# Optimization experiments

Measured on AMD Instinct MI355X. Metric: run time of the kernel, lower is better.

## Reference

```python
import jax, jax.numpy as jnp
import numpy as np

DIM = 96       # d_model / channels
DSTATE = 16    # SSM state size N
DINNER = 2 * DIM   # expand=2 -> 192
DTRANK = 6     # ceil(DIM/16)
K = 4          # scan directions
B, H, W = 2, 56, 56


def _ln(x, g, b, eps=1e-5):
    m = x.mean(-1, keepdims=True)
    v = x.var(-1, keepdims=True)
    return (x - m) * jax.lax.rsqrt(v + eps) * g + b


def _dwconv3(x, w, b):  # x [B,C,H,W], w [C,1,3,3] depthwise, SAME padding
    y = jax.lax.conv_general_dilated(x, w, (1, 1), [(1, 1), (1, 1)],
                                     feature_group_count=x.shape[1],
                                     dimension_numbers=('NCHW', 'OIHW', 'NCHW'))
    return y + b[None, :, None, None]


def _bn(x, g, b, m, v, eps=1e-5):  # eval-mode BatchNorm2d on NCHW
    inv = jax.lax.rsqrt(v + eps)
    return (x - m[None, :, None, None]) * (inv * g)[None, :, None, None] + b[None, :, None, None]


def _selective_scan(u, dt, A, Bs, Cs, Dp, dt_bias):
    # u, dt: [B,K,D,L]; A: [K,D,N]; Bs,Cs: [B,K,N,L]; Dp, dt_bias: [K,D]
    dt = jax.nn.softplus(dt + dt_bias[None, :, :, None])
    dA = jnp.exp(jnp.einsum('bkdl,kdn->lbkdn', dt, A))           # [L,B,K,D,N]
    dBu = jnp.einsum('bkdl,bknl,bkdl->lbkdn', dt, Bs, u)          # [L,B,K,D,N]
    Ct = jnp.moveaxis(Cs, -1, 0)                                  # [L,B,K,N]
    h0 = jnp.zeros(dA.shape[1:], dA.dtype)

    def step(h, inp):
        dA_l, dBu_l, C_l = inp
        h = dA_l * h + dBu_l
        return h, jnp.einsum('bkdn,bkn->bkd', h, C_l)

    _, ys = jax.lax.scan(step, h0, (dA, dBu, Ct))                 # ys [L,B,K,D]
    return jnp.moveaxis(ys, 0, -1) + u * Dp[None, :, :, None]     # [B,K,D,L]


def setup_inputs() -> dict:
    key = jax.random.key(0)
    ks = jax.random.split(key, 12)
    s = 0.02
    f32 = jnp.float32
    inp = {}
    inp['x'] = jax.random.normal(ks[0], (B, H, W, DIM), f32)
    # conv branch: depthwise 3x3 + BN + ReLU + 1x1 + BN
    inp['dw_w'] = jax.random.normal(ks[1], (DIM, 1, 3, 3), f32) * s
    inp['dw_b'] = jnp.zeros((DIM,), f32)
    inp['bn1_g'] = jnp.ones((DIM,), f32); inp['bn1_b'] = jnp.zeros((DIM,), f32)
    inp['bn1_m'] = jnp.zeros((DIM,), f32); inp['bn1_v'] = jnp.ones((DIM,), f32)
    inp['pw_w'] = jax.random.normal(ks[2], (DIM, DIM), f32) * s
    inp['pw_b'] = jnp.zeros((DIM,), f32)
    inp['bn2_g'] = jnp.ones((DIM,), f32); inp['bn2_b'] = jnp.zeros((DIM,), f32)
    inp['bn2_m'] = jnp.zeros((DIM,), f32); inp['bn2_v'] = jnp.ones((DIM,), f32)
    # pre-mamba LayerNorm
    inp['ln_g'] = jnp.ones((DIM,), f32); inp['ln_b'] = jnp.zeros((DIM,), f32)
    # SS2D params
    inp['in_proj_w'] = jax.random.normal(ks[3], (2 * DINNER, DIM), f32) * s
    inp['conv_w'] = jax.random.normal(ks[4], (DINNER, 1, 3, 3), f32) * s
    inp['conv_b'] = jnp.zeros((DINNER,), f32)
    inp['x_proj_w'] = jax.random.normal(ks[5], (K, DTRANK + 2 * DSTATE, DINNER), f32) * s
    inp['dt_w'] = jax.random.normal(ks[6], (K, DINNER, DTRANK), f32) * s
    inp['dt_b'] = jnp.full((K, DINNER), -4.6, f32)  # softplus(dt_b) ~= 0.01
    inp['A_logs'] = jnp.log(jnp.tile(jnp.arange(1, DSTATE + 1, dtype=f32), (K * DINNER, 1)))
    inp['Ds'] = jnp.ones((K * DINNER,), f32)
    inp['out_norm_g'] = jnp.ones((DINNER,), f32); inp['out_norm_b'] = jnp.zeros((DINNER,), f32)
    inp['out_proj_w'] = jax.random.normal(ks[7], (DIM, DINNER), f32) * s
    # fusion: Linear(2*dim, dim) + LayerNorm(dim)
    inp['fus_w'] = jax.random.normal(ks[8], (DIM, 2 * DIM), f32) * s
    inp['fus_b'] = jnp.zeros((DIM,), f32)
    inp['fus_ln_g'] = jnp.ones((DIM,), f32); inp['fus_ln_b'] = jnp.zeros((DIM,), f32)
    return inp


def reference(x, dw_w, dw_b, bn1_g, bn1_b, bn1_m, bn1_v, pw_w, pw_b,
              bn2_g, bn2_b, bn2_m, bn2_v, ln_g, ln_b,
              in_proj_w, conv_w, conv_b, x_proj_w, dt_w, dt_b, A_logs, Ds,
              out_norm_g, out_norm_b, out_proj_w, fus_w, fus_b, fus_ln_g, fus_ln_b):
    Bsz, Hh, Ww, C = x.shape
    L = Hh * Ww
    # ----- conv branch -----
    xc = jnp.transpose(x, (0, 3, 1, 2))                       # [B,C,H,W]
    c = jax.nn.relu(_bn(_dwconv3(xc, dw_w, dw_b), bn1_g, bn1_b, bn1_m, bn1_v))
    c = jnp.einsum('bchw,oc->bohw', c, pw_w) + pw_b[None, :, None, None]
    conv_out = jnp.transpose(_bn(c, bn2_g, bn2_b, bn2_m, bn2_v), (0, 2, 3, 1))
    # ----- mamba (SS2D) branch -----
    xn = _ln(x, ln_g, ln_b)
    xz = xn @ in_proj_w.T                                     # [B,H,W,2*Din]
    xm, z = jnp.split(xz, 2, axis=-1)
    xm = jnp.transpose(xm, (0, 3, 1, 2))                      # [B,Din,H,W]
    xm = jax.nn.silu(_dwconv3(xm, conv_w, conv_b))
    v1 = xm.reshape(Bsz, DINNER, L)                           # row-major scan
    v2 = jnp.transpose(xm, (0, 1, 3, 2)).reshape(Bsz, DINNER, L)  # col-major scan
    xs = jnp.stack([v1, v2, v1[..., ::-1], v2[..., ::-1]], axis=1)  # [B,4,Din,L]
    x_dbl = jnp.einsum('bkdl,kcd->bkcl', xs, x_proj_w)
    dts, Bmat, Cmat = jnp.split(x_dbl, [DTRANK, DTRANK + DSTATE], axis=2)
    dts = jnp.einsum('bkrl,kdr->bkdl', dts, dt_w)
    A = -jnp.exp(A_logs).reshape(K, DINNER, DSTATE)
    out_y = _selective_scan(xs, dts, A, Bmat, Cmat, Ds.reshape(K, DINNER), dt_b)
    y1 = out_y[:, 0]
    inv_y = out_y[:, 2:4][..., ::-1]
    y2 = inv_y[:, 0]
    y3 = jnp.transpose(inv_y[:, 1].reshape(Bsz, DINNER, Ww, Hh), (0, 1, 3, 2)).reshape(Bsz, DINNER, L)
    y4 = jnp.transpose(out_y[:, 1].reshape(Bsz, DINNER, Ww, Hh), (0, 1, 3, 2)).reshape(Bsz, DINNER, L)
    y = jnp.transpose(y1 + y2 + y3 + y4, (0, 2, 1)).reshape(Bsz, Hh, Ww, DINNER)
    y = _ln(y, out_norm_g, out_norm_b)
    y = y * jax.nn.silu(z)
    mamba_out = y @ out_proj_w.T                              # [B,H,W,C]
    # ----- fusion + residual -----
    fused = jnp.concatenate([conv_out, mamba_out], axis=-1) @ fus_w.T + fus_b
    fused = _ln(fused, fus_ln_g, fus_ln_b)
    return x + fused
```

## Files before the change

kernel.cpp:

```cpp
#include <hip/hip_runtime.h>
#include <math.h>

#define BZ 2
#define HH 56
#define WW 56
#define LL 3136
#define CC 96
#define DI 192
#define NS 16
#define RR 6
#define NT 49
#define NCH 98
#define CH 32

#define OFF_CONV   0
#define OFF_XMRAW  602112
#define OFF_Z      1806336
#define OFF_V1     3010560
#define OFF_V2     4214784
#define OFF_DT     5419008
#define OFF_BS     10235904
#define OFF_CS     10637312
#define OFF_Y      11038720
#define OFF_Y13    15855616
#define OFF_T      18264064
#define OFF_W2     19468288

__device__ __forceinline__ float softplusf(float x) {
    if (x > 20.f) return x;
    return log1pf(__expf(x));
}

__global__ __launch_bounds__(64) void k0_w2(const float* __restrict__ fus_w,
                                            const float* __restrict__ opw,
                                            float* __restrict__ W2) {
    int i = blockIdx.x * 64 + threadIdx.x;
    if (i >= CC * DI) return;
    int o = i / DI, d = i % DI;
    float acc = 0.f;
    for (int j = 0; j < CC; ++j)
        acc += fus_w[o * DI + CC + j] * opw[j * DI + d];
    W2[i] = acc;
}

__global__ __launch_bounds__(256) void k0c_negA(const float* __restrict__ A_logs,
                                                float* __restrict__ negA) {
    int i = blockIdx.x * 256 + threadIdx.x;
    if (i < 4 * DI * NS) negA[i] = -__expf(A_logs[i]);
}

__global__ __launch_bounds__(256) void k1a_dw(const float* __restrict__ x,
    const float* __restrict__ dw_w, const float* __restrict__ dw_b,
    const float* __restrict__ bn1_g, const float* __restrict__ bn1_b,
    const float* __restrict__ bn1_m, const float* __restrict__ bn1_v,
    float* __restrict__ cbuf) {
    int i = blockIdx.x * 256 + threadIdx.x;
    if (i >= BZ * LL * CC) return;
    int c = i % CC;
    int bl = i / CC;
    int l = bl % LL, b = bl / LL;
    int h = l / WW, w = l % WW;
    float acc = dw_b[c];
    #pragma unroll
    for (int dy = -1; dy <= 1; ++dy) {
        int hh = h + dy; if (hh < 0 || hh >= HH) continue;
        #pragma unroll
        for (int dx = -1; dx <= 1; ++dx) {
            int ww = w + dx; if (ww < 0 || ww >= WW) continue;
            acc += x[((b * HH + hh) * WW + ww) * CC + c] * dw_w[c * 9 + (dy + 1) * 3 + (dx + 1)];
        }
    }
    float inv = rsqrtf(bn1_v[c] + 1e-5f);
    float v = (acc - bn1_m[c]) * inv * bn1_g[c] + bn1_b[c];
    cbuf[i] = fmaxf(v, 0.f);
}

__global__ __launch_bounds__(256) void k1b_pw(const float* __restrict__ cbuf,
    const float* __restrict__ pw_w, const float* __restrict__ pw_b,
    const float* __restrict__ bn2_g, const float* __restrict__ bn2_b,
    const float* __restrict__ bn2_m, const float* __restrict__ bn2_v,
    float* __restrict__ conv_out) {
    int t0 = blockIdx.x * 64;
    int b = blockIdx.y;
    int lane = threadIdx.x & 63;
    int wvu = __builtin_amdgcn_readfirstlane(threadIdx.x >> 6);
    __shared__ float ct[CC * 65];
    __shared__ float res[64 * 97];
    const float* cb = cbuf + (b * LL + t0) * CC;
    for (int e = threadIdx.x; e < 64 * CC; e += 256) {
        int p = e / CC, c = e % CC;
        ct[c * 65 + p] = cb[e];
    }
    __syncthreads();
    float acc[24];
    const float* pb = pw_b + wvu * 24;
    #pragma unroll
    for (int j = 0; j < 24; ++j) acc[j] = pb[j];
    const float* wb = pw_w + (wvu * 24) * CC;
    for (int c = 0; c < CC; ++c) {
        float xv = ct[c * 65 + lane];
        #pragma unroll
        for (int j = 0; j < 24; ++j)
            acc[j] += xv * wb[j * CC + c];
    }
    #pragma unroll
    for (int j = 0; j < 24; ++j) {
        int o = wvu * 24 + j;
        float inv = rsqrtf(bn2_v[o] + 1e-5f);
        res[lane * 97 + o] = (acc[j] - bn2_m[o]) * inv * bn2_g[o] + bn2_b[o];
    }
    __syncthreads();
    float* ob = conv_out + (b * LL + t0) * CC;
    for (int e = threadIdx.x; e < 64 * CC; e += 256) {
        int pl = e / CC, o = e % CC;
        ob[e] = res[pl * 97 + o];
    }
}

__global__ __launch_bounds__(256) void k2_inproj(const float* __restrict__ x,
    const float* __restrict__ ln_g, const float* __restrict__ ln_b,
    const float* __restrict__ ipw,
    float* __restrict__ xm_raw, float* __restrict__ z_buf) {
    int t0 = blockIdx.x * 64;
    int og = blockIdx.y;
    int b = blockIdx.z;
    int lane = threadIdx.x & 63;
    int wv = threadIdx.x >> 6;
    int wvu = __builtin_amdgcn_readfirstlane(wv);
    __shared__ float xt[64 * 97];
    __shared__ float xn[96 * 65];
    __shared__ float ps[4][64], ps2[4][64];
    const float* xb = x + (b * LL + t0) * CC;
    for (int e = threadIdx.x; e < 64 * CC; e += 256) {
        int p = e / CC, c = e % CC;
        xt[p * 97 + c] = xb[e];
    }
    __syncthreads();
    float s = 0.f, s2 = 0.f;
    #pragma unroll
    for (int j = 0; j < 24; ++j) {
        float v = xt[lane * 97 + wvu * 24 + j];
        s += v; s2 += v * v;
    }
    ps[wv][lane] = s; ps2[wv][lane] = s2;
    __syncthreads();
    float st = 0.f, st2 = 0.f;
    #pragma unroll
    for (int i = 0; i < 4; ++i) { st += ps[i][lane]; st2 += ps2[i][lane]; }
    float m = st * (1.f / 96.f);
    float inv = rsqrtf(st2 * (1.f / 96.f) - m * m + 1e-5f);
    #pragma unroll
    for (int j = 0; j < 24; ++j) {
        int c = wvu * 24 + j;
        xn[c * 65 + lane] = (xt[lane * 97 + c] - m) * inv * ln_g[c] + ln_b[c];
    }
    __syncthreads();
    float acc[24];
    #pragma unroll
    for (int j = 0; j < 24; ++j) acc[j] = 0.f;
    const float* wbase = ipw + (og * 96 + wvu * 24) * CC;
    for (int c = 0; c < CC; ++c) {
        float xv = xn[c * 65 + lane];
        #pragma unroll
        for (int j = 0; j < 24; ++j)
            acc[j] += xv * wbase[j * CC + c];
    }
    int p = t0 + lane;
    #pragma unroll
    for (int j = 0; j < 24; ++j) {
        int out = og * 96 + wvu * 24 + j;
        if (out < DI) xm_raw[(b * DI + out) * LL + p] = acc[j];
        else          z_buf[(b * DI + (out - DI)) * LL + p] = acc[j];
    }
}

__global__ __launch_bounds__(256) void k3_dw(const float* __restrict__ xm_raw,
    const float* __restrict__ conv_w, const float* __restrict__ conv_b,
    float* __restrict__ v1, float* __restrict__ v2) {
    int bd = blockIdx.x;
    int half = blockIdx.y;
    int d = bd % DI;
    int h0 = half * 28;
    __shared__ float tile[28 * 57];
    const float* src = xm_raw + bd * LL;
    float wloc[9];
    #pragma unroll
    for (int i = 0; i < 9; ++i) wloc[i] = conv_w[d * 9 + i];
    float bias = conv_b[d];
    for (int e = threadIdx.x; e < 28 * WW; e += 256) {
        int hl = e / WW, w = e % WW;
        int h = h0 + hl;
        float acc = bias;
        #pragma unroll
        for (int dy = -1; dy <= 1; ++dy) {
            int hh = h + dy; if (hh < 0 || hh >= HH) continue;
            #pragma unroll
            for (int dx = -1; dx <= 1; ++dx) {
                int ww = w + dx; if (ww < 0 || ww >= WW) continue;
                acc += src[hh * WW + ww] * wloc[(dy + 1) * 3 + (dx + 1)];
            }
        }
        float sig = 1.f / (1.f + __expf(-acc));
        float v = acc * sig;
        v1[bd * LL + h * WW + w] = v;
        tile[hl * 57 + w] = v;
    }
    __syncthreads();
    for (int e = threadIdx.x; e < 28 * WW; e += 256) {
        int w = e / 28, hl = e % 28;
        v2[bd * LL + w * HH + h0 + hl] = tile[hl * 57 + w];
    }
}

__global__ __launch_bounds__(256) void k4_proj(const float* __restrict__ v1,
    const float* __restrict__ v2, const float* __restrict__ xpw,
    const float* __restrict__ dtw, const float* __restrict__ dtb,
    float* __restrict__ dt_s, float* __restrict__ B_s, float* __restrict__ C_s) {
    int t0 = blockIdx.x * 64;
    int k = blockIdx.y;
    int b = blockIdx.z;
    int lane = threadIdx.x & 63;
    int wvu = __builtin_amdgcn_readfirstlane(threadIdx.x >> 6);
    __shared__ float xs_l[DI * 64];
    __shared__ float dtr[RR * 64];
    const float* src = ((k & 1) == 0 ? v1 : v2) + b * DI * LL + t0;
    for (int e = threadIdx.x; e < DI * 64; e += 256) {
        int d = e >> 6, p = e & 63;
        xs_l[e] = src[d * LL + p];
    }
    __syncthreads();
    int r0 = wvu * 10; if (r0 > 28) r0 = 28;
    float acc[10];
    #pragma unroll
    for (int i = 0; i < 10; ++i) acc[i] = 0.f;
    const float* wbase = xpw + (k * 38 + r0) * DI;
    for (int d = 0; d < DI; ++d) {
        float xv = xs_l[d * 64 + lane];
        #pragma unroll
        for (int i = 0; i < 10; ++i)
            acc[i] += xv * wbase[i * DI + d];
    }
    int p = t0 + lane;
    #pragma unroll
    for (int i = 0; i < 10; ++i) {
        int c = r0 + i;
        if (c < RR) {
            dtr[c * 64 + lane] = acc[i];
        } else if (c < RR + NS) {
            B_s[((b * 4 + k) * NS + (c - RR)) * LL + p] = acc[i];
        } else {
            C_s[((b * 4 + k) * NS + (c - RR - NS)) * LL + p] = acc[i];
        }
    }
    __syncthreads();
    for (int i = 0; i < 48; ++i) {
        int d = wvu * 48 + i;
        float a = dtb[k * DI + d];
        const float* wr = dtw + (k * DI + d) * RR;
        #pragma unroll
        for (int r = 0; r < RR; ++r)
            a += dtr[r * 64 + lane] * wr[r];
        dt_s[((b * 4 + k) * DI + d) * LL + p] = softplusf(a);
    }
}

__global__ __launch_bounds__(64) void k5a_scan(const float* __restrict__ dt_s,
    const float* __restrict__ B_s, const float* __restrict__ C_s,
    const float* __restrict__ v1, const float* __restrict__ v2,
    const float* __restrict__ A_logs, float* __restrict__ y_scan,
    float* __restrict__ hl_buf, float* __restrict__ Tbuf) {
    int bx = blockIdx.x;
    int dg = bx % 3, c = bx / 3;
    int k = blockIdx.y, b = blockIdx.z;
    int bk = b * 4 + k;
    int lane = threadIdx.x;
    int d0 = dg * 64, d = d0 + lane;
    bool fwd = (k < 2);
    int s0 = fwd ? c * CH : (LL - (c + 1) * CH);
    __shared__ float dtl[64 * 33];
    __shared__ float ul[64 * 33];
    __shared__ float bc[CH * 36];
    float Ae[16];
    const float* ap = A_logs + (k * DI + d) * NS;
    #pragma unroll
    for (int n = 0; n < 16; ++n) Ae[n] = -__expf(ap[n]) * 1.442695040888963f;
    const float* dtp = dt_s + (bk * DI + d0) * LL + s0;
    const float* up  = ((k & 1) == 0 ? v1 : v2) + (b * DI + d0) * LL + s0;
    int pr = lane >> 5, pc = lane & 31;
    #pragma unroll 8
    for (int i = 0; i < 32; ++i) {
        int row = i * 2 + pr;
        dtl[row * 33 + pc] = dtp[row * LL + pc];
        ul[row * 33 + pc]  = up[row * LL + pc];
    }
    #pragma unroll
    for (int i = 0; i < 8; ++i) {
        int nn = i * 2 + pr;
        bc[pc * 36 + nn]      = B_s[(bk * NS + nn) * LL + s0 + pc];
        bc[pc * 36 + 16 + nn] = C_s[(bk * NS + nn) * LL + s0 + pc];
    }
    __syncthreads();
    float h[16];
    #pragma unroll
    for (int n = 0; n < 16; ++n) h[n] = 0.f;
    float cum = 0.f;
    for (int jj = 0; jj < CH; ++jj) {
        int j = fwd ? jj : CH - 1 - jj;
        float dtv = dtl[lane * 33 + j];
        float uv  = ul[lane * 33 + j];
        float du = dtv * uv;
        cum += dtv;
        const float4* row4 = (const float4*)&bc[j * 36];
        float4 b0 = row4[0], b1 = row4[1], b2 = row4[2], b3 = row4[3];
        float4 c0 = row4[4], c1 = row4[5], c2 = row4[6], c3 = row4[7];
        float bv[16] = {b0.x,b0.y,b0.z,b0.w, b1.x,b1.y,b1.z,b1.w,
                        b2.x,b2.y,b2.z,b2.w, b3.x,b3.y,b3.z,b3.w};
        float cv[16] = {c0.x,c0.y,c0.z,c0.w, c1.x,c1.y,c1.z,c1.w,
                        c2.x,c2.y,c2.z,c2.w, c3.x,c3.y,c3.z,c3.w};
        float y = 0.f;
        #pragma unroll
        for (int n = 0; n < 16; ++n) {
            h[n] = exp2f(dtv * Ae[n]) * h[n] + du * bv[n];
            y += h[n] * cv[n];
        }
        ul[lane * 33 + j] = y;
    }
    __syncthreads();
    float* yp = y_scan + (bk * DI + d0) * LL + s0;
    #pragma unroll 8
    for (int i = 0; i < 32; ++i) {
        int row = i * 2 + pr;
        yp[row * LL + pc] = ul[row * 33 + pc];
    }
    float4* hp4 = (float4*)(hl_buf + (bk * NCH + c) * (DI * NS) + d * NS);
    hp4[0] = make_float4(h[0], h[1], h[2], h[3]);
    hp4[1] = make_float4(h[4], h[5], h[6], h[7]);
    hp4[2] = make_float4(h[8], h[9], h[10], h[11]);
    hp4[3] = make_float4(h[12], h[13], h[14], h[15]);
    Tbuf[(bk * NCH + c) * DI + d] = cum;
}

__global__ __launch_bounds__(64) void k5c_comb(float* __restrict__ hl_buf,
    const float* __restrict__ Tbuf, const float* __restrict__ negA) {
    int dg = blockIdx.x, k = blockIdx.y, b = blockIdx.z;
    int lane = threadIdx.x, dl = lane >> 4, n = lane & 15;
    int d = dg * 4 + dl;
    int bk = b * 4 + k;
    float Av = negA[(k * DI + d) * NS + n];
    float H = 0.f;
    for (int c = 0; c < NCH; ++c) {
        float* slot = hl_buf + (bk * NCH + c) * (DI * NS) + dg * 64 + lane;
        float hl = *slot;
        *slot = H;
        float T = Tbuf[(bk * NCH + c) * DI + d];
        H = hl + __expf(Av * T) * H;
    }
}

__global__ __launch_bounds__(256) void k5d_corr(const float* __restrict__ dt_s,
    const float* __restrict__ C_s, const float* __restrict__ hin,
    const float* __restrict__ negA, float* __restrict__ y_scan) {
    int t = blockIdx.x;
    int k = blockIdx.y, b = blockIdx.z;
    bool fwd = (k < 2);
    int c  = fwd ? (t + 1) : (NCH - 1 - t);
    int s0 = fwd ? (t + 1) * CH : t * CH;
    int p32 = threadIdx.x & 31, sl = threadIdx.x >> 5;
    int bk = b * 4 + k;
    __shared__ float c_l[16 * 33];
    for (int e = threadIdx.x; e < 16 * CH; e += 256) {
        int n = e >> 5, s = e & 31;
        c_l[n * 33 + s] = C_s[(bk * NS + n) * LL + s0 + s];
    }
    __syncthreads();
    for (int j = 0; j < 24; ++j) {
        int d = sl * 24 + j;
        float dtv = dt_s[(bk * DI + d) * LL + s0 + p32];
        float cum = dtv;
        if (fwd) {
            #pragma unroll
            for (int off = 1; off < 32; off <<= 1) {
                float o = __shfl_up(cum, off, 32);
                if (p32 >= off) cum += o;
            }
        } else {
            #pragma unroll
            for (int off = 1; off < 32; off <<= 1) {
                float o = __shfl_down(cum, off, 32);
                if (p32 < 32 - off) cum += o;
            }
        }
        const float* hp = hin + (bk * NCH + c) * (DI * NS) + d * 16;
        const float* ap = negA + (k * DI + d) * NS;
        float acc = 0.f;
        #pragma unroll
        for (int n = 0; n < 16; ++n) {
            acc += c_l[n * 33 + p32] * __expf(ap[n] * cum) * hp[n];
        }
        y_scan[(bk * DI + d) * LL + s0 + p32] += acc;
    }
}

__global__ __launch_bounds__(256) void k5b_tr(const float* __restrict__ y_scan,
                                              float* __restrict__ y13t) {
    int idx = blockIdx.x;
    int d = idx % DI;
    int bk = idx / DI;
    int kk = bk % 2, b = bk / 2;
    int k = (kk == 0) ? 1 : 3;
    __shared__ float tile[HH * 57];
    const float* src = y_scan + ((b * 4 + k) * DI + d) * LL;
    for (int e = threadIdx.x; e < LL; e += 256) {
        int w = e / HH, h = e % HH;
        tile[h * 57 + w] = src[e];
    }
    __syncthreads();
    float* dst = y13t + idx * LL;
    for (int e = threadIdx.x; e < LL; e += 256) {
        int h = e / WW, w = e % WW;
        dst[e] = tile[h * 57 + w];
    }
}

__global__ __launch_bounds__(256) void k6_gather(const float* __restrict__ y_scan,
    const float* __restrict__ y13t, const float* __restrict__ v1,
    const float* __restrict__ z_buf, const float* __restrict__ Ds,
    const float* __restrict__ ong, const float* __restrict__ onb,
    float* __restrict__ t_buf) {
    int t0 = blockIdx.x * 32;
    int b = blockIdx.y;
    int p32 = threadIdx.x & 31, sl = threadIdx.x >> 5;
    int p = t0 + p32;
    __shared__ float yv[DI * 33];
    __shared__ float ps[8][32], ps2[8][32];
    float s = 0.f, s2 = 0.f;
    for (int j = 0; j < 24; ++j) {
        int d = sl * 24 + j;
        float dsum = Ds[d] + Ds[DI + d] + Ds[2 * DI + d] + Ds[3 * DI + d];
        float val = y_scan[((b * 4 + 0) * DI + d) * LL + p]
                  + y_scan[((b * 4 + 2) * DI + d) * LL + p]
                  + y13t[((b * 2 + 0) * DI + d) * LL + p]
                  + y13t[((b * 2 + 1) * DI + d) * LL + p]
                  + v1[(b * DI + d) * LL + p] * dsum;
        yv[d * 33 + p32] = val;
        s += val; s2 += val * val;
    }
    ps[sl][p32] = s; ps2[sl][p32] = s2;
    __syncthreads();
    float st = 0.f, st2 = 0.f;
    #pragma unroll
    for (int i = 0; i < 8; ++i) { st += ps[i][p32]; st2 += ps2[i][p32]; }
    float m = st * (1.f / 192.f);
    float inv = rsqrtf(st2 * (1.f / 192.f) - m * m + 1e-5f);
    for (int j = 0; j < 24; ++j) {
        int d = sl * 24 + j;
        float val = (yv[d * 33 + p32] - m) * inv * ong[d] + onb[d];
        float zz = z_buf[(b * DI + d) * LL + p];
        float sig = 1.f / (1.f + __expf(-zz));
        t_buf[(b * DI + d) * LL + p] = val * zz * sig;
    }
}

__global__ __launch_bounds__(256) void k7a_mm(const float* __restrict__ t_buf,
    const float* __restrict__ conv_out, const float* __restrict__ W2,
    const float* __restrict__ fus_w, const float* __restrict__ fus_b,
    float* __restrict__ fusedT) {
    int t0 = blockIdx.x * 64;
    int og = blockIdx.y;
    int b = blockIdx.z;
    int lane = threadIdx.x & 63;
    int wvu = __builtin_amdgcn_readfirstlane(threadIdx.x >> 6);
    __shared__ float ct[CC * 65];
    const float* cb = conv_out + (b * LL + t0) * CC;
    for (int e = threadIdx.x; e < 64 * CC; e += 256) {
        int p = e / CC, c = e % CC;
        ct[c * 65 + p] = cb[e];
    }
    __syncthreads();
    int o0 = og * 24 + wvu * 6;
    float acc[6];
    #pragma unroll
    for (int j = 0; j < 6; ++j) acc[j] = fus_b[o0 + j];
    int p = t0 + lane;
    const float* w2 = W2 + o0 * DI;
    for (int d = 0; d < DI; ++d) {
        float tv = t_buf[(b * DI + d) * LL + p];
        #pragma unroll
        for (int j = 0; j < 6; ++j)
            acc[j] += tv * w2[j * DI + d];
    }
    const float* fw = fus_w + o0 * DI;
    for (int c = 0; c < CC; ++c) {
        float cv = ct[c * 65 + lane];
        #pragma unroll
        for (int j = 0; j < 6; ++j)
            acc[j] += cv * fw[j * DI + c];
    }
    #pragma unroll
    for (int j = 0; j < 6; ++j)
        fusedT[(b * CC + o0 + j) * LL + p] = acc[j];
}

__global__ __launch_bounds__(256) void k7b_ln(const float* __restrict__ fusedT,
    const float* __restrict__ flg, const float* __restrict__ flb,
    const float* __restrict__ x, float* __restrict__ out) {
    int t0 = blockIdx.x * 64;
    int b = blockIdx.y;
    int lane = threadIdx.x & 63, wv = threadIdx.x >> 6;
    __shared__ float ft[CC * 65];
    __shared__ float res[64 * 97];
    __shared__ float ps[4][64], ps2[4][64];
    for (int e = threadIdx.x; e < CC * 64; e += 256) {
        int o = e >> 6, p = e & 63;
        ft[o * 65 + p] = fusedT[(b * CC + o) * LL + t0 + p];
    }
    __syncthreads();
    float s = 0.f, s2 = 0.f;
    #pragma unroll
    for (int j = 0; j < 24; ++j) {
        float v = ft[(wv * 24 + j) * 65 + lane];
        s += v; s2 += v * v;
    }
    ps[wv][lane] = s; ps2[wv][lane] = s2;
    __syncthreads();
    float st = 0.f, st2 = 0.f;
    #pragma unroll
    for (int i = 0; i < 4; ++i) { st += ps[i][lane]; st2 += ps2[i][lane]; }
    float m = st * (1.f / 96.f);
    float inv = rsqrtf(st2 * (1.f / 96.f) - m * m + 1e-5f);
    #pragma unroll
    for (int j = 0; j < 24; ++j) {
        int o = wv * 24 + j;
        res[lane * 97 + o] = (ft[o * 65 + lane] - m) * inv * flg[o] + flb[o];
    }
    __syncthreads();
    const float* xb = x + (b * LL + t0) * CC;
    float* ob = out + (b * LL + t0) * CC;
    for (int e = threadIdx.x; e < 64 * CC; e += 256) {
        int pl = e / CC, o = e % CC;
        ob[e] = xb[e] + res[pl * 97 + o];
    }
}

extern "C" void kernel_launch(void* const* d_in, const int* in_sizes, int n_in,
                              void* d_out, int out_size, void* d_ws, size_t ws_size,
                              hipStream_t stream) {
    const float* x        = (const float*)d_in[0];
    const float* dw_w     = (const float*)d_in[1];
    const float* dw_b     = (const float*)d_in[2];
    const float* bn1_g    = (const float*)d_in[3];
    const float* bn1_b    = (const float*)d_in[4];
    const float* bn1_m    = (const float*)d_in[5];
    const float* bn1_v    = (const float*)d_in[6];
    const float* pw_w     = (const float*)d_in[7];
    const float* pw_b     = (const float*)d_in[8];
    const float* bn2_g    = (const float*)d_in[9];
    const float* bn2_b    = (const float*)d_in[10];
    const float* bn2_m    = (const float*)d_in[11];
    const float* bn2_v    = (const float*)d_in[12];
    const float* ln_g     = (const float*)d_in[13];
    const float* ln_b     = (const float*)d_in[14];
    const float* ipw      = (const float*)d_in[15];
    const float* conv_w   = (const float*)d_in[16];
    const float* conv_b   = (const float*)d_in[17];
    const float* xpw      = (const float*)d_in[18];
    const float* dtw      = (const float*)d_in[19];
    const float* dtb      = (const float*)d_in[20];
    const float* A_logs   = (const float*)d_in[21];
    const float* Ds       = (const float*)d_in[22];
    const float* ong      = (const float*)d_in[23];
    const float* onb      = (const float*)d_in[24];
    const float* opw      = (const float*)d_in[25];
    const float* fus_w    = (const float*)d_in[26];
    const float* fus_b    = (const float*)d_in[27];
    const float* flg      = (const float*)d_in[28];
    const float* flb      = (const float*)d_in[29];

    float* ws = (float*)d_ws;
    float* conv_out = ws + OFF_CONV;
    float* xm_raw   = ws + OFF_XMRAW;
    float* z_buf    = ws + OFF_Z;
    float* v1       = ws + OFF_V1;
    float* v2       = ws + OFF_V2;
    float* dt_s     = ws + OFF_DT;
    float* B_s      = ws + OFF_BS;
    float* C_s      = ws + OFF_CS;
    float* y_scan   = ws + OFF_Y;
    float* y13t     = ws + OFF_Y13;
    float* t_buf    = ws + OFF_T;
    float* W2       = ws + OFF_W2;
    float* cbuf     = y13t;
    float* hl_buf   = y13t;
    float* Tbuf     = xm_raw;
    float* negA     = B_s;
    float* fusedT   = y13t;
    float* out      = (float*)d_out;

    k0_w2<<<dim3((CC * DI + 63) / 64), dim3(64), 0, stream>>>(fus_w, opw, W2);
    k1a_dw<<<dim3((BZ * LL * CC + 255) / 256), dim3(256), 0, stream>>>(x, dw_w, dw_b,
                                                     bn1_g, bn1_b, bn1_m, bn1_v, cbuf);
    k1b_pw<<<dim3(NT, BZ), dim3(256), 0, stream>>>(cbuf, pw_w, pw_b,
                                                   bn2_g, bn2_b, bn2_m, bn2_v, conv_out);
    k2_inproj<<<dim3(NT, 4, BZ), dim3(256), 0, stream>>>(x, ln_g, ln_b, ipw, xm_raw, z_buf);
    k3_dw<<<dim3(BZ * DI, 2), dim3(256), 0, stream>>>(xm_raw, conv_w, conv_b, v1, v2);
    k4_proj<<<dim3(NT, 4, BZ), dim3(256), 0, stream>>>(v1, v2, xpw, dtw, dtb, dt_s, B_s, C_s);
    k5a_scan<<<dim3(3 * NCH, 4, BZ), dim3(64), 0, stream>>>(dt_s, B_s, C_s, v1, v2, A_logs,
                                                            y_scan, hl_buf, Tbuf);
    k0c_negA<<<dim3(48), dim3(256), 0, stream>>>(A_logs, negA);
    k5c_comb<<<dim3(48, 4, BZ), dim3(64), 0, stream>>>(hl_buf, Tbuf, negA);
    k5d_corr<<<dim3(NCH - 1, 4, BZ), dim3(256), 0, stream>>>(dt_s, C_s, hl_buf, negA, y_scan);
    k5b_tr<<<dim3(BZ * 2 * DI), dim3(256), 0, stream>>>(y_scan, y13t);
    k6_gather<<<dim3(2 * NT, BZ), dim3(256), 0, stream>>>(y_scan, y13t, v1, z_buf, Ds, ong, onb, t_buf);
    k7a_mm<<<dim3(NT, 4, BZ), dim3(256), 0, stream>>>(t_buf, conv_out, W2, fus_w, fus_b, fusedT);
    k7b_ln<<<dim3(NT, BZ), dim3(256), 0, stream>>>(fusedT, flg, flb, x, out);
}
```

Measured before the change: 372.0 us.

## Split GEMM and LN kernels into more blocks and register-cache scan chunks

Halves per-thread output work in the in-projection, x-projection and fusion matmul kernels and shrinks the token tiles in the gather and final LayerNorm kernels, so each launch has more blocks to spread across the GPU. The scan kernel is templated on direction and split into forward and backward launches. Each thread now keeps its own 32-step dt/u chunk in registers, loaded and stored as float4, instead of staging it through shared memory. The chunk-combine loop prefetches the next chunk's state. The cost is recomputing LN and reloading inputs in more blocks, plus higher register pressure in the scan.

```diff
diff --git a/kernel.cpp b/kernel.cpp
--- a/kernel.cpp
+++ b/kernel.cpp
@@ -155,20 +155,21 @@
         xn[c * 65 + lane] = (xt[lane * 97 + c] - m) * inv * ln_g[c] + ln_b[c];
     }
     __syncthreads();
-    float acc[24];
-    #pragma unroll
-    for (int j = 0; j < 24; ++j) acc[j] = 0.f;
-    const float* wbase = ipw + (og * 96 + wvu * 24) * CC;
+    float acc[12];
+    #pragma unroll
+    for (int j = 0; j < 12; ++j) acc[j] = 0.f;
+    int o0 = og * 48 + wvu * 12;
+    const float* wbase = ipw + o0 * CC;
     for (int c = 0; c < CC; ++c) {
         float xv = xn[c * 65 + lane];
         #pragma unroll
-        for (int j = 0; j < 24; ++j)
+        for (int j = 0; j < 12; ++j)
             acc[j] += xv * wbase[j * CC + c];
     }
     int p = t0 + lane;
     #pragma unroll
-    for (int j = 0; j < 24; ++j) {
-        int out = og * 96 + wvu * 24 + j;
+    for (int j = 0; j < 12; ++j) {
+        int out = o0 + j;
         if (out < DI) xm_raw[(b * DI + out) * LL + p] = acc[j];
         else          z_buf[(b * DI + (out - DI)) * LL + p] = acc[j];
     }
@@ -217,7 +218,8 @@
     const float* __restrict__ dtw, const float* __restrict__ dtb,
     float* __restrict__ dt_s, float* __restrict__ B_s, float* __restrict__ C_s) {
     int t0 = blockIdx.x * 64;
-    int k = blockIdx.y;
+    int ky = blockIdx.y;
+    int k = ky >> 1, half = ky & 1;
     int b = blockIdx.z;
     int lane = threadIdx.x & 63;
     int wvu = __builtin_amdgcn_readfirstlane(threadIdx.x >> 6);
@@ -229,20 +231,21 @@
         xs_l[e] = src[d * LL + p];
     }
     __syncthreads();
-    int r0 = wvu * 10; if (r0 > 28) r0 = 28;
-    float acc[10];
-    #pragma unroll
-    for (int i = 0; i < 10; ++i) acc[i] = 0.f;
+    int rl = wvu * 5; if (rl > 14) rl = 14;
+    int r0 = half * 19 + rl;
+    float acc[5];
+    #pragma unroll
+    for (int i = 0; i < 5; ++i) acc[i] = 0.f;
     const float* wbase = xpw + (k * 38 + r0) * DI;
     for (int d = 0; d < DI; ++d) {
         float xv = xs_l[d * 64 + lane];
         #pragma unroll
-        for (int i = 0; i < 10; ++i)
+        for (int i = 0; i < 5; ++i)
             acc[i] += xv * wbase[i * DI + d];
     }
     int p = t0 + lane;
     #pragma unroll
-    for (int i = 0; i < 10; ++i) {
+    for (int i = 0; i < 5; ++i) {
         int c = r0 + i;
         if (c < RR) {
             dtr[c * 64 + lane] = acc[i];
@@ -253,46 +256,46 @@
         }
     }
     __syncthreads();
-    for (int i = 0; i < 48; ++i) {
-        int d = wvu * 48 + i;
-        float a = dtb[k * DI + d];
-        const float* wr = dtw + (k * DI + d) * RR;
-        #pragma unroll
-        for (int r = 0; r < RR; ++r)
-            a += dtr[r * 64 + lane] * wr[r];
-        dt_s[((b * 4 + k) * DI + d) * LL + p] = softplusf(a);
-    }
-}
-
-__global__ __launch_bounds__(64) void k5a_scan(const float* __restrict__ dt_s,
+    if (half == 0) {
+        for (int i = 0; i < 48; ++i) {
+            int d = wvu * 48 + i;
+            float a = dtb[k * DI + d];
+            const float* wr = dtw + (k * DI + d) * RR;
+            #pragma unroll
+            for (int r = 0; r < RR; ++r)
+                a += dtr[r * 64 + lane] * wr[r];
+            dt_s[((b * 4 + k) * DI + d) * LL + p] = softplusf(a);
+        }
+    }
+}
+
+template<bool FWD>
+__global__ __launch_bounds__(64, 2) void k5a_scan(const float* __restrict__ dt_s,
     const float* __restrict__ B_s, const float* __restrict__ C_s,
     const float* __restrict__ v1, const float* __restrict__ v2,
     const float* __restrict__ A_logs, float* __restrict__ y_scan,
-    float* __restrict__ hl_buf, float* __restrict__ Tbuf) {
+    float* __restrict__ hl_buf, float* __restrict__ Tbuf, int kbase) {
     int bx = blockIdx.x;
     int dg = bx % 3, c = bx / 3;
-    int k = blockIdx.y, b = blockIdx.z;
+    int k = kbase + blockIdx.y;
+    int b = blockIdx.z;
     int bk = b * 4 + k;
     int lane = threadIdx.x;
     int d0 = dg * 64, d = d0 + lane;
-    bool fwd = (k < 2);
-    int s0 = fwd ? c * CH : (LL - (c + 1) * CH);
-    __shared__ float dtl[64 * 33];
-    __shared__ float ul[64 * 33];
+    int s0 = FWD ? c * CH : (LL - (c + 1) * CH);
     __shared__ float bc[CH * 36];
     float Ae[16];
     const float* ap = A_logs + (k * DI + d) * NS;
     #pragma unroll
     for (int n = 0; n < 16; ++n) Ae[n] = -__expf(ap[n]) * 1.442695040888963f;
-    const float* dtp = dt_s + (bk * DI + d0) * LL + s0;
-    const float* up  = ((k & 1) == 0 ? v1 : v2) + (b * DI + d0) * LL + s0;
+    const float4* dtp4 = (const float4*)(dt_s + (bk * DI + d) * LL + s0);
+    const float4* up4  = (const float4*)((((k & 1) == 0) ? v1 : v2) + (b * DI + d) * LL + s0);
+    float4 dt4[8], u4[8];
+    #pragma unroll
+    for (int i = 0; i < 8; ++i) { dt4[i] = dtp4[i]; u4[i] = up4[i]; }
+    float* dts = (float*)dt4;
+    float* us  = (float*)u4;
     int pr = lane >> 5, pc = lane & 31;
-    #pragma unroll 8
-    for (int i = 0; i < 32; ++i) {
-        int row = i * 2 + pr;
-        dtl[row * 33 + pc] = dtp[row * LL + pc];
-        ul[row * 33 + pc]  = up[row * LL + pc];
-    }
     #pragma unroll
     for (int i = 0; i < 8; ++i) {
         int nn = i * 2 + pr;
@@ -304,10 +307,11 @@
     #pragma unroll
     for (int n = 0; n < 16; ++n) h[n] = 0.f;
     float cum = 0.f;
+    #pragma unroll
     for (int jj = 0; jj < CH; ++jj) {
-        int j = fwd ? jj : CH - 1 - jj;
-        float dtv = dtl[lane * 33 + j];
-        float uv  = ul[lane * 33 + j];
+        const int j = FWD ? jj : CH - 1 - jj;
+        float dtv = dts[j];
+        float uv  = us[j];
         float du = dtv * uv;
         cum += dtv;
         const float4* row4 = (const float4*)&bc[j * 36];
@@ -323,15 +327,11 @@
             h[n] = exp2f(dtv * Ae[n]) * h[n] + du * bv[n];
             y += h[n] * cv[n];
         }
-        ul[lane * 33 + j] = y;
-    }
-    __syncthreads();
-    float* yp = y_scan + (bk * DI + d0) * LL + s0;
-    #pragma unroll 8
-    for (int i = 0; i < 32; ++i) {
-        int row = i * 2 + pr;
-        yp[row * LL + pc] = ul[row * 33 + pc];
-    }
+        us[j] = y;
+    }
+    float4* yp4 = (float4*)(y_scan + (bk * DI + d) * LL + s0);
+    #pragma unroll
+    for (int i = 0; i < 8; ++i) yp4[i] = u4[i];
     float4* hp4 = (float4*)(hl_buf + (bk * NCH + c) * (DI * NS) + d * NS);
     hp4[0] = make_float4(h[0], h[1], h[2], h[3]);
     hp4[1] = make_float4(h[4], h[5], h[6], h[7]);
@@ -348,11 +348,16 @@
     int bk = b * 4 + k;
     float Av = negA[(k * DI + d) * NS + n];
     float H = 0.f;
+    float* slot0 = hl_buf + (bk * NCH + 0) * (DI * NS) + dg * 64 + lane;
+    float hl_next = *slot0;
+    float T_next = Tbuf[(bk * NCH + 0) * DI + d];
     for (int c = 0; c < NCH; ++c) {
-        float* slot = hl_buf + (bk * NCH + c) * (DI * NS) + dg * 64 + lane;
-        float hl = *slot;
-        *slot = H;
-        float T = Tbuf[(bk * NCH + c) * DI + d];
+        float hl = hl_next, T = T_next;
+        if (c + 1 < NCH) {
+            hl_next = hl_buf[(bk * NCH + c + 1) * (DI * NS) + dg * 64 + lane];
+            T_next  = Tbuf[(bk * NCH + c + 1) * DI + d];
+        }
+        hl_buf[(bk * NCH + c) * (DI * NS) + dg * 64 + lane] = H;
         H = hl + __expf(Av * T) * H;
     }
 }
@@ -427,34 +432,34 @@
     const float* __restrict__ z_buf, const float* __restrict__ Ds,
     const float* __restrict__ ong, const float* __restrict__ onb,
     float* __restrict__ t_buf) {
-    int t0 = blockIdx.x * 32;
+    int t0 = blockIdx.x * 16;
     int b = blockIdx.y;
-    int p32 = threadIdx.x & 31, sl = threadIdx.x >> 5;
-    int p = t0 + p32;
-    __shared__ float yv[DI * 33];
-    __shared__ float ps[8][32], ps2[8][32];
+    int p16 = threadIdx.x & 15, sl = threadIdx.x >> 4;
+    int p = t0 + p16;
+    __shared__ float yv[DI * 17];
+    __shared__ float ps[16][16], ps2[16][16];
     float s = 0.f, s2 = 0.f;
-    for (int j = 0; j < 24; ++j) {
-        int d = sl * 24 + j;
+    for (int j = 0; j < 12; ++j) {
+        int d = sl * 12 + j;
         float dsum = Ds[d] + Ds[DI + d] + Ds[2 * DI + d] + Ds[3 * DI + d];
         float val = y_scan[((b * 4 + 0) * DI + d) * LL + p]
                   + y_scan[((b * 4 + 2) * DI + d) * LL + p]
                   + y13t[((b * 2 + 0) * DI + d) * LL + p]
                   + y13t[((b * 2 + 1) * DI + d) * LL + p]
                   + v1[(b * DI + d) * LL + p] * dsum;
-        yv[d * 33 + p32] = val;
+        yv[d * 17 + p16] = val;
         s += val; s2 += val * val;
     }
-    ps[sl][p32] = s; ps2[sl][p32] = s2;
+    ps[sl][p16] = s; ps2[sl][p16] = s2;
     __syncthreads();
     float st = 0.f, st2 = 0.f;
     #pragma unroll
-    for (int i = 0; i < 8; ++i) { st += ps[i][p32]; st2 += ps2[i][p32]; }
+    for (int i = 0; i < 16; ++i) { st += ps[i][p16]; st2 += ps2[i][p16]; }
     float m = st * (1.f / 192.f);
     float inv = rsqrtf(st2 * (1.f / 192.f) - m * m + 1e-5f);
-    for (int j = 0; j < 24; ++j) {
-        int d = sl * 24 + j;
-        float val = (yv[d * 33 + p32] - m) * inv * ong[d] + onb[d];
+    for (int j = 0; j < 12; ++j) {
+        int d = sl * 12 + j;
+        float val = (yv[d * 17 + p16] - m) * inv * ong[d] + onb[d];
         float zz = z_buf[(b * DI + d) * LL + p];
         float sig = 1.f / (1.f + __expf(-zz));
         t_buf[(b * DI + d) * LL + p] = val * zz * sig;
@@ -477,66 +482,66 @@
         ct[c * 65 + p] = cb[e];
     }
     __syncthreads();
-    int o0 = og * 24 + wvu * 6;
-    float acc[6];
-    #pragma unroll
-    for (int j = 0; j < 6; ++j) acc[j] = fus_b[o0 + j];
+    int o0 = og * 12 + wvu * 3;
+    float acc[3];
+    #pragma unroll
+    for (int j = 0; j < 3; ++j) acc[j] = fus_b[o0 + j];
     int p = t0 + lane;
     const float* w2 = W2 + o0 * DI;
     for (int d = 0; d < DI; ++d) {
         float tv = t_buf[(b * DI + d) * LL + p];
         #pragma unroll
-        for (int j = 0; j < 6; ++j)
+        for (int j = 0; j < 3; ++j)
             acc[j] += tv * w2[j * DI + d];
     }
     const float* fw = fus_w + o0 * DI;
     for (int c = 0; c < CC; ++c) {
         float cv = ct[c * 65 + lane];
         #pragma unroll
-        for (int j = 0; j < 6; ++j)
+        for (int j = 0; j < 3; ++j)
             acc[j] += cv * fw[j * DI + c];
     }
     #pragma unroll
-    for (int j = 0; j < 6; ++j)
+    for (int j = 0; j < 3; ++j)
         fusedT[(b * CC + o0 + j) * LL + p] = acc[j];
 }
 
 __global__ __launch_bounds__(256) void k7b_ln(const float* __restrict__ fusedT,
     const float* __restrict__ flg, const float* __restrict__ flb,
     const float* __restrict__ x, float* __restrict__ out) {
-    int t0 = blockIdx.x * 64;
+    int t0 = blockIdx.x * 16;
     int b = blockIdx.y;
-    int lane = threadIdx.x & 63, wv = threadIdx.x >> 6;
-    __shared__ float ft[CC * 65];
-    __shared__ float res[64 * 97];
-    __shared__ float ps[4][64], ps2[4][64];
-    for (int e = threadIdx.x; e < CC * 64; e += 256) {
-        int o = e >> 6, p = e & 63;
-        ft[o * 65 + p] = fusedT[(b * CC + o) * LL + t0 + p];
+    int p16 = threadIdx.x & 15, sl = threadIdx.x >> 4;
+    __shared__ float ft[CC * 17];
+    __shared__ float res[16 * 97];
+    __shared__ float ps[16][16], ps2[16][16];
+    for (int e = threadIdx.x; e < CC * 16; e += 256) {
+        int o = e >> 4, p = e & 15;
+        ft[o * 17 + p] = fusedT[(b * CC + o) * LL + t0 + p];
     }
     __syncthreads();
     float s = 0.f, s2 = 0.f;
     #pragma unroll
-    for (int j = 0; j < 24; ++j) {
-        float v = ft[(wv * 24 + j) * 65 + lane];
+    for (int j = 0; j < 6; ++j) {
+        float v = ft[(sl * 6 + j) * 17 + p16];
         s += v; s2 += v * v;
     }
-    ps[wv][lane] = s; ps2[wv][lane] = s2;
+    ps[sl][p16] = s; ps2[sl][p16] = s2;
     __syncthreads();
     float st = 0.f, st2 = 0.f;
     #pragma unroll
-    for (int i = 0; i < 4; ++i) { st += ps[i][lane]; st2 += ps2[i][lane]; }
+    for (int i = 0; i < 16; ++i) { st += ps[i][p16]; st2 += ps2[i][p16]; }
     float m = st * (1.f / 96.f);
     float inv = rsqrtf(st2 * (1.f / 96.f) - m * m + 1e-5f);
     #pragma unroll
-    for (int j = 0; j < 24; ++j) {
-        int o = wv * 24 + j;
-        res[lane * 97 + o] = (ft[o * 65 + lane] - m) * inv * flg[o] + flb[o];
+    for (int j = 0; j < 6; ++j) {
+        int o = sl * 6 + j;
+        res[p16 * 97 + o] = (ft[o * 17 + p16] - m) * inv * flg[o] + flb[o];
     }
     __syncthreads();
     const float* xb = x + (b * LL + t0) * CC;
     float* ob = out + (b * LL + t0) * CC;
-    for (int e = threadIdx.x; e < 64 * CC; e += 256) {
+    for (int e = threadIdx.x; e < 16 * CC; e += 256) {
         int pl = e / CC, o = e % CC;
         ob[e] = xb[e] + res[pl * 97 + o];
     }
@@ -601,16 +606,18 @@
                                                      bn1_g, bn1_b, bn1_m, bn1_v, cbuf);
     k1b_pw<<<dim3(NT, BZ), dim3(256), 0, stream>>>(cbuf, pw_w, pw_b,
                                                    bn2_g, bn2_b, bn2_m, bn2_v, conv_out);
-    k2_inproj<<<dim3(NT, 4, BZ), dim3(256), 0, stream>>>(x, ln_g, ln_b, ipw, xm_raw, z_buf);
+    k2_inproj<<<dim3(NT, 8, BZ), dim3(256), 0, stream>>>(x, ln_g, ln_b, ipw, xm_raw, z_buf);
     k3_dw<<<dim3(BZ * DI, 2), dim3(256), 0, stream>>>(xm_raw, conv_w, conv_b, v1, v2);
-    k4_proj<<<dim3(NT, 4, BZ), dim3(256), 0, stream>>>(v1, v2, xpw, dtw, dtb, dt_s, B_s, C_s);
-    k5a_scan<<<dim3(3 * NCH, 4, BZ), dim3(64), 0, stream>>>(dt_s, B_s, C_s, v1, v2, A_logs,
-                                                            y_scan, hl_buf, Tbuf);
+    k4_proj<<<dim3(NT, 8, BZ), dim3(256), 0, stream>>>(v1, v2, xpw, dtw, dtb, dt_s, B_s, C_s);
+    k5a_scan<true><<<dim3(3 * NCH, 2, BZ), dim3(64), 0, stream>>>(dt_s, B_s, C_s, v1, v2, A_logs,
+                                                            y_scan, hl_buf, Tbuf, 0);
+    k5a_scan<false><<<dim3(3 * NCH, 2, BZ), dim3(64), 0, stream>>>(dt_s, B_s, C_s, v1, v2, A_logs,
+                                                            y_scan, hl_buf, Tbuf, 2);
     k0c_negA<<<dim3(48), dim3(256), 0, stream>>>(A_logs, negA);
     k5c_comb<<<dim3(48, 4, BZ), dim3(64), 0, stream>>>(hl_buf, Tbuf, negA);
     k5d_corr<<<dim3(NCH - 1, 4, BZ), dim3(256), 0, stream>>>(dt_s, C_s, hl_buf, negA, y_scan);
     k5b_tr<<<dim3(BZ * 2 * DI), dim3(256), 0, stream>>>(y_scan, y13t);
-    k6_gather<<<dim3(2 * NT, BZ), dim3(256), 0, stream>>>(y_scan, y13t, v1, z_buf, Ds, ong, onb, t_buf);
-    k7a_mm<<<dim3(NT, 4, BZ), dim3(256), 0, stream>>>(t_buf, conv_out, W2, fus_w, fus_b, fusedT);
-    k7b_ln<<<dim3(NT, BZ), dim3(256), 0, stream>>>(fusedT, flg, flb, x, out);
-}
+    k6_gather<<<dim3(196, BZ), dim3(256), 0, stream>>>(y_scan, y13t, v1, z_buf, Ds, ong, onb, t_buf);
+    k7a_mm<<<dim3(NT, 8, BZ), dim3(256), 0, stream>>>(t_buf, conv_out, W2, fus_w, fus_b, fusedT);
+    k7b_ln<<<dim3(196, BZ), dim3(256), 0, stream>>>(fusedT, flg, flb, x, out);
+}
```

Result: no change. 379.1 us (+1.9%).
